# Optimization experiments

Measured on AMD Instinct MI355X. Metric: run time of the kernel, lower is better.

The kernel has to match this reference:

```python
import jax, jax.numpy as jnp
import numpy as np
jax.config.update("jax_enable_x64", True)  # RoPE is applied in float64 in the original

NH, NKV, HD, ROT = 32, 8, 64, 32


def _rope(x, cos, sin):
    # x: [B,h,S,HD]; cos/sin: [B,1,S,ROT//2] (float64)
    x = x.astype(jnp.float64)
    x_rot, x_pass = x[..., :ROT], x[..., ROT:]
    r, i = x_rot[..., :ROT // 2], x_rot[..., ROT // 2:]
    o_r = r * cos - i * sin
    o_i = r * sin + i * cos
    out = jnp.stack((o_r, o_i), axis=-1).reshape(x.shape[:-1] + (ROT,))
    return jnp.concatenate([out, x_pass], axis=-1)


def setup_inputs() -> dict:
    key = jax.random.key(0)
    ks = jax.random.split(key, 16)
    B, S, H, I = 1, 2048, 2048, 8192
    f = jnp.float32
    s = 0.02
    qkv_dim = NH * HD + 2 * NKV * HD  # 3072
    d = {}
    d["hidden_states"] = jax.random.normal(ks[0], (B, S, H), f)
    d["position_ids"] = jnp.arange(B * S, dtype=jnp.int64).reshape(B, S)
    d["cos"] = jax.random.uniform(ks[1], (B, 1, S, ROT // 2), f)
    d["sin"] = jax.random.uniform(ks[2], (B, 1, S, ROT // 2), f)
    d["ln_w"] = jnp.ones((H,), f)
    d["ln_b"] = jnp.zeros((H,), f)
    d["wq"] = jax.random.normal(ks[3], (H, NH * HD), f) * s
    d["wk"] = jax.random.normal(ks[4], (H, NKV * HD), f) * s
    d["wv"] = jax.random.normal(ks[5], (H, NKV * HD), f) * s
    d["wo"] = jax.random.normal(ks[6], (NH * HD, H), f) * s
    d["tau_wq"] = jax.random.normal(ks[7], (qkv_dim, NH), f) * s
    d["tau_wv"] = jax.random.normal(ks[8], (qkv_dim, NH), f) * s
    d["tau_alpha"] = jax.random.normal(ks[9], (NH,), f) * s
    d["up_w"] = jax.random.normal(ks[10], (H, I), f) * s
    d["up_b"] = jnp.zeros((I,), f)
    d["down_w"] = jax.random.normal(ks[11], (I, H), f) * s
    d["down_b"] = jnp.zeros((H,), f)
    return d


def reference(hidden_states, position_ids, cos, sin, ln_w, ln_b, wq, wk, wv, wo,
              tau_wq, tau_wv, tau_alpha, up_w, up_b, down_w, down_b):
    B, S, H = hidden_states.shape
    eps = 1e-5
    # input_layernorm (shared by parallel attn + mlp branches)
    mu = hidden_states.mean(-1, keepdims=True)
    var = hidden_states.var(-1, keepdims=True)
    xn = (hidden_states - mu) / jnp.sqrt(var + eps) * ln_w + ln_b

    # ---- attention with tau gating ----
    q = xn @ wq          # [B,S,NH*HD]
    k = xn @ wk          # [B,S,NKV*HD]
    v = xn @ wv
    qkv = jnp.concatenate([q, k, v], axis=-1)
    tok = jax.nn.gelu(qkv, approximate=False)  # F.gelu default (erf)
    tok_q = jnp.tanh(tok @ tau_wq).transpose(0, 2, 1)  # [B,NH,S]
    tok_v = jnp.tanh(tok @ tau_wv).transpose(0, 2, 1)
    pos = position_ids.astype(tok_q.dtype) + 1
    tau_pos = 1 + (jax.nn.sigmoid(tau_alpha[None, :, None] * jnp.log(pos)[:, None, :]) - 0.5)
    tau_q = (tok_q + tau_pos)[..., None]  # [B,NH,S,1]
    tau_v = (tok_v + tau_pos)[..., None]

    qh = q.reshape(B, S, NH, HD).transpose(0, 2, 1, 3) * tau_q
    kh = k.reshape(B, S, NKV, HD).transpose(0, 2, 1, 3)
    vh = v.reshape(B, S, NKV, HD).transpose(0, 2, 1, 3) * tau_v[:, :NKV]  # repeat-then-slice == first NKV heads

    cos64 = cos.astype(jnp.float64)
    sin64 = sin.astype(jnp.float64)
    qh = _rope(qh, cos64, sin64).astype(jnp.float32)
    kh = _rope(kh, cos64, sin64).astype(jnp.float32)

    g = NH // NKV
    kh = jnp.repeat(kh, g, axis=1)  # GQA expand [B,NKV,S,D] -> [B,NH,S,D]
    vh = jnp.repeat(vh, g, axis=1)

    scores = jnp.einsum('bhqd,bhkd->bhqk', qh, kh) / jnp.sqrt(jnp.float32(HD))
    causal = jnp.tril(jnp.ones((S, S), dtype=bool))
    scores = jnp.where(causal, scores, jnp.float32(-1e9))
    p = jax.nn.softmax(scores, axis=-1)
    attn = jnp.einsum('bhqk,bhkd->bhqd', p, vh)
    attn = attn.transpose(0, 2, 1, 3).reshape(B, S, NH * HD)
    attn_out = attn @ wo

    # ---- dense MLP (gelu_pytorch_tanh, ungated) ----
    h = jax.nn.gelu(xn @ up_w + up_b, approximate=True)
    mlp_out = h @ down_w + down_b

    return hidden_states + attn_out + mlp_out
```

## Files before the change

kernel.cpp:

```cpp
#include <hip/hip_runtime.h>
#include <hip/hip_bf16.h>
#include <math.h>

typedef __bf16 bf16;
typedef bf16 bf16x4 __attribute__((ext_vector_type(4)));
typedef bf16 bf16x8 __attribute__((ext_vector_type(8)));
typedef float f32x4 __attribute__((ext_vector_type(4)));

#define AS1 __attribute__((address_space(1)))
#define AS3 __attribute__((address_space(3)))

__global__ __launch_bounds__(256) void k_transpose(const float* __restrict__ src,
                                                   bf16* __restrict__ dst,
                                                   int R, int C, int dstStride) {
    __shared__ float tile[32][33];
    int bc = blockIdx.x * 32, br = blockIdx.y * 32;
    int tx = threadIdx.x & 31, ty = threadIdx.x >> 5;
    for (int i = 0; i < 4; i++) {
        int r = ty + i * 8;
        tile[r][tx] = src[(size_t)(br + r) * C + bc + tx];
    }
    __syncthreads();
    for (int i = 0; i < 4; i++) {
        int r = ty + i * 8;
        dst[(size_t)(bc + r) * dstStride + br + tx] = (bf16)tile[tx][r];
    }
}

__global__ __launch_bounds__(256) void k_ln(const float* __restrict__ x,
                                            const float* __restrict__ w,
                                            const float* __restrict__ b,
                                            bf16* __restrict__ xn) {
    int s = blockIdx.x;
    int t = threadIdx.x;
    const float* row = x + (size_t)s * 2048;
    const float4* r4 = (const float4*)row;
    float4 A = r4[t * 2], B = r4[t * 2 + 1];
    float sum = A.x + A.y + A.z + A.w + B.x + B.y + B.z + B.w;
    float sq = A.x * A.x + A.y * A.y + A.z * A.z + A.w * A.w +
               B.x * B.x + B.y * B.y + B.z * B.z + B.w * B.w;
    for (int off = 32; off; off >>= 1) {
        sum += __shfl_down(sum, off);
        sq  += __shfl_down(sq, off);
    }
    __shared__ float rs[4], rq[4];
    if ((t & 63) == 0) { rs[t >> 6] = sum; rq[t >> 6] = sq; }
    __syncthreads();
    float S = rs[0] + rs[1] + rs[2] + rs[3];
    float Q = rq[0] + rq[1] + rq[2] + rq[3];
    float mu = S * (1.0f / 2048.0f);
    float var = Q * (1.0f / 2048.0f) - mu * mu;
    float rstd = rsqrtf(var + 1e-5f);
    float vals[8] = {A.x, A.y, A.z, A.w, B.x, B.y, B.z, B.w};
    bf16x8 ov;
    int j0 = t * 8;
    for (int i = 0; i < 8; i++)
        ov[i] = (bf16)((vals[i] - mu) * rstd * w[j0 + i] + b[j0 + i]);
    *(bf16x8*)&xn[(size_t)s * 2048 + j0] = ov;
}

template <int MODE>
__global__ __launch_bounds__(256) void k_gemm(const bf16* __restrict__ A,
                                              const bf16* __restrict__ Bt,
                                              int M, int N, int K, int kslice,
                                              float* __restrict__ Cf,
                                              bf16* __restrict__ Cb,
                                              const float* __restrict__ bias) {
    __shared__ bf16 As[2][128][64];
    __shared__ bf16 Bs[2][128][64];
    int t = threadIdx.x;
    int bm = blockIdx.y, bn = blockIdx.x, bz = blockIdx.z;
    int w = t >> 6, l = t & 63, lr = l & 15, lg = l >> 4;
    int wm = w >> 1, wn = w & 1;
    f32x4 acc[4][4] = {};
    const bf16* Ab = A + (size_t)(bm * 128) * K + (size_t)bz * kslice;
    const bf16* Bb = Bt + (size_t)(bn * 128) * K + (size_t)bz * kslice;
    int srow = t >> 3;
    int scol = ((t & 7) ^ (srow & 7)) * 8;
    int nkt = kslice >> 6;

    auto STAGE = [&](int kt, int buf) {
        int k0 = kt * 64;
#pragma unroll
        for (int i = 0; i < 4; i++) {
            const bf16* ga = Ab + (size_t)(i * 32 + srow) * K + k0 + scol;
            const bf16* gb = Bb + (size_t)(i * 32 + srow) * K + k0 + scol;
            char* la = (char*)(&As[buf][0][0]) + i * 4096 + w * 1024;
            char* lb = (char*)(&Bs[buf][0][0]) + i * 4096 + w * 1024;
            __builtin_amdgcn_global_load_lds(
                (const AS1 void*)ga, (AS3 void*)la, 16, 0, 0);
            __builtin_amdgcn_global_load_lds(
                (const AS1 void*)gb, (AS3 void*)lb, 16, 0, 0);
        }
    };

    int sw = (lr & 7) << 4;

    STAGE(0, 0);
    for (int kt = 0; kt < nkt; ++kt) {
        int cur = kt & 1;
        if (kt + 1 < nkt) {
            STAGE(kt + 1, cur ^ 1);
            asm volatile("s_waitcnt vmcnt(8) lgkmcnt(0)" ::: "memory");
        } else {
            asm volatile("s_waitcnt vmcnt(0) lgkmcnt(0)" ::: "memory");
        }
        __builtin_amdgcn_s_barrier();
        asm volatile("" ::: "memory");
        const char* Abase = (const char*)&As[cur][0][0];
        const char* Bbase = (const char*)&Bs[cur][0][0];
#pragma unroll
        for (int kk = 0; kk < 2; kk++) {
            bf16x8 a[4], b[4];
            for (int fm = 0; fm < 4; fm++)
                a[fm] = *(const bf16x8*)(Abase + (wm * 64 + fm * 16 + lr) * 128 +
                                         ((kk * 64 + lg * 16) ^ sw));
            for (int fn = 0; fn < 4; fn++)
                b[fn] = *(const bf16x8*)(Bbase + (wn * 64 + fn * 16 + lr) * 128 +
                                         ((kk * 64 + lg * 16) ^ sw));
            for (int fm = 0; fm < 4; fm++)
                for (int fn = 0; fn < 4; fn++)
                    acc[fm][fn] = __builtin_amdgcn_mfma_f32_16x16x32_bf16(
                        a[fm], b[fn], acc[fm][fn], 0, 0, 0);
        }
        asm volatile("" ::: "memory");
        __builtin_amdgcn_s_barrier();
    }
    float* Cz = Cf + (size_t)bz * M * N;
    for (int fm = 0; fm < 4; fm++)
        for (int fn = 0; fn < 4; fn++) {
            int col = bn * 128 + wn * 64 + fn * 16 + lr;
            for (int r = 0; r < 4; r++) {
                int row = bm * 128 + wm * 64 + fm * 16 + lg * 4 + r;
                size_t idx = (size_t)row * N + col;
                float v = acc[fm][fn][r];
                if constexpr (MODE == 0) {
                    Cz[idx] = v;
                } else {
                    v += bias[col];
                    float e = __expf(1.5957691216057308f * (v + 0.044715f * v * v * v));
                    float th = 1.0f - 2.0f / (e + 1.0f);
                    Cb[idx] = (bf16)(0.5f * v * (1.0f + th));
                }
            }
        }
}

template <int MODE>
__global__ __launch_bounds__(512, 2) void k_gemm256(const bf16* __restrict__ A,
                                                    const bf16* __restrict__ Bt,
                                                    int M, int N, int K, int kslice,
                                                    float* __restrict__ Cf,
                                                    float* __restrict__ Cf2,
                                                    bf16* __restrict__ Cb,
                                                    const float* __restrict__ bias) {
    __shared__ bf16 As[2][256][64];
    __shared__ bf16 Bs[2][256][64];
    int t = threadIdx.x;
    int w = t >> 6, l = t & 63, lr = l & 15, lg = l >> 4;
    int wm = w >> 2, wn = w & 3;
    int bm = blockIdx.y, bn = blockIdx.x, bz = blockIdx.z;
    f32x4 acc[8][4] = {};
    const bf16* Ab = A + (size_t)(bm * 256) * K + (size_t)bz * kslice;
    const bf16* Bb = Bt + (size_t)(bn * 256) * K + (size_t)bz * kslice;
    int srow = t >> 3;
    int scol = ((t & 7) ^ (srow & 7)) * 8;
    int nkt = kslice >> 6;
    int sw = (lr & 7) << 4;

    auto STAGE = [&](int kt, int buf) {
        int k0 = kt * 64;
#pragma unroll
        for (int i = 0; i < 4; i++) {
            const bf16* ga = Ab + (size_t)(i * 64 + srow) * K + k0 + scol;
            const bf16* gb = Bb + (size_t)(i * 64 + srow) * K + k0 + scol;
            char* la = (char*)(&As[buf][0][0]) + (i * 64 + w * 8) * 128;
            char* lb = (char*)(&Bs[buf][0][0]) + (i * 64 + w * 8) * 128;
            __builtin_amdgcn_global_load_lds(
                (const AS1 void*)ga, (AS3 void*)la, 16, 0, 0);
            __builtin_amdgcn_global_load_lds(
                (const AS1 void*)gb, (AS3 void*)lb, 16, 0, 0);
        }
    };

    STAGE(0, 0);
    asm volatile("s_waitcnt vmcnt(0)" ::: "memory");
    __builtin_amdgcn_s_barrier();
    asm volatile("" ::: "memory");

    for (int kt = 0; kt < nkt; ++kt) {
        int cur = kt & 1;
        const char* Abase = (const char*)&As[cur][0][0] + (wm * 128) * 128;
        const char* Bbase = (const char*)&Bs[cur][0][0] + (wn * 64) * 128;
        bf16x8 a[4][2], b[2][2];
#pragma unroll
        for (int ph = 0; ph < 4; ++ph) {
            const int qm = ph >> 1;
            const int qn = (ph == 1 || ph == 2) ? 1 : 0;
            if (ph == 0 || ph == 2) {
#pragma unroll
                for (int fm = 0; fm < 4; fm++)
#pragma unroll
                    for (int kk = 0; kk < 2; kk++)
                        a[fm][kk] = *(const bf16x8*)(Abase +
                            (qm * 64 + fm * 16 + lr) * 128 +
                            ((kk * 64 + lg * 16) ^ sw));
            }
            if (ph != 2) {
#pragma unroll
                for (int fn = 0; fn < 2; fn++)
#pragma unroll
                    for (int kk = 0; kk < 2; kk++)
                        b[fn][kk] = *(const bf16x8*)(Bbase +
                            (qn * 32 + fn * 16 + lr) * 128 +
                            ((kk * 64 + lg * 16) ^ sw));
            }
            if (ph == 0 && kt + 1 < nkt) STAGE(kt + 1, cur ^ 1);
            __builtin_amdgcn_s_barrier();
            asm volatile("s_waitcnt lgkmcnt(0)" ::: "memory");
            __builtin_amdgcn_sched_barrier(0);
            __builtin_amdgcn_s_setprio(1);
#pragma unroll
            for (int fm = 0; fm < 4; fm++)
#pragma unroll
                for (int fn = 0; fn < 2; fn++)
#pragma unroll
                    for (int kk = 0; kk < 2; kk++)
                        acc[qm * 4 + fm][qn * 2 + fn] =
                            __builtin_amdgcn_mfma_f32_16x16x32_bf16(
                                a[fm][kk], b[fn][kk],
                                acc[qm * 4 + fm][qn * 2 + fn], 0, 0, 0);
            __builtin_amdgcn_s_setprio(0);
            if (ph == 3) asm volatile("s_waitcnt vmcnt(0)" ::: "memory");
            asm volatile("" ::: "memory");
            __builtin_amdgcn_s_barrier();
        }
    }

    float* Cz = ((bz < 2) ? Cf : Cf2) + (size_t)(bz & 1) * M * N;
#pragma unroll
    for (int mi = 0; mi < 8; mi++)
#pragma unroll
        for (int ni = 0; ni < 4; ni++) {
            int col = bn * 256 + wn * 64 + (ni >> 1) * 32 + (ni & 1) * 16 + lr;
            for (int r = 0; r < 4; r++) {
                int row = bm * 256 + wm * 128 + (mi >> 2) * 64 + (mi & 3) * 16 +
                          lg * 4 + r;
                size_t idx = (size_t)row * N + col;
                float v = acc[mi][ni][r];
                if constexpr (MODE == 0) {
                    Cz[idx] = v;
                } else {
                    v += bias[col];
                    float e = __expf(1.5957691216057308f * (v + 0.044715f * v * v * v));
                    float th = 1.0f - 2.0f / (e + 1.0f);
                    Cb[idx] = (bf16)(0.5f * v * (1.0f + th));
                }
            }
        }
}

__global__ __launch_bounds__(256) void k_final(const float* __restrict__ hidden,
                                               const float* __restrict__ w0,
                                               const float* __restrict__ w1,
                                               const float* __restrict__ p0,
                                               const float* __restrict__ p1,
                                               const float* __restrict__ p2,
                                               const float* __restrict__ p3,
                                               const float* __restrict__ bias,
                                               float* __restrict__ out) {
    int idx = blockIdx.x * 256 + threadIdx.x;
    int col4 = idx & 511;
    float4 b = ((const float4*)bias)[col4];
    float4 h = ((const float4*)hidden)[idx];
    float4 a0 = ((const float4*)w0)[idx];
    float4 a1 = ((const float4*)w1)[idx];
    float4 d0 = ((const float4*)p0)[idx];
    float4 d1 = ((const float4*)p1)[idx];
    float4 d2 = ((const float4*)p2)[idx];
    float4 d3 = ((const float4*)p3)[idx];
    float4 o;
    o.x = h.x + a0.x + a1.x + d0.x + d1.x + d2.x + d3.x + b.x;
    o.y = h.y + a0.y + a1.y + d0.y + d1.y + d2.y + d3.y + b.y;
    o.z = h.z + a0.z + a1.z + d0.z + d1.z + d2.z + d3.z + b.z;
    o.w = h.w + a0.w + a1.w + d0.w + d1.w + d2.w + d3.w + b.w;
    ((float4*)out)[idx] = o;
}

__global__ __launch_bounds__(256) void k_tau(const float* __restrict__ qkv,
                                             const float* __restrict__ twq,
                                             const float* __restrict__ twv,
                                             const float* __restrict__ alpha,
                                             const int* __restrict__ pos,
                                             float* __restrict__ tauq,
                                             float* __restrict__ tauv) {
    int s = blockIdx.x;
    __shared__ float tok[3072];
    __shared__ float part[4][64];
    const float* row = qkv + (size_t)s * 3072;
    for (int j = threadIdx.x; j < 3072; j += 256) {
        float x = row[j];
        tok[j] = x * 0.5f * (1.0f + erff(x * 0.7071067811865475f));
    }
    __syncthreads();
    int h = threadIdx.x & 63;
    int chunk = threadIdx.x >> 6;
    const float* W = (h < 32) ? twq : twv;
    int hh = h & 31;
    float acc = 0.0f;
    int j0 = chunk * 768;
    for (int j = j0; j < j0 + 768; ++j) acc += tok[j] * W[j * 32 + hh];
    part[chunk][h] = acc;
    __syncthreads();
    if (chunk == 0) {
        float tot = part[0][h] + part[1][h] + part[2][h] + part[3][h];
        float pf = (float)(pos[s] + 1);
        float lp = logf(pf);
        float tp = 1.0f + (1.0f / (1.0f + expf(-alpha[hh] * lp)) - 0.5f);
        float val = tanhf(tot) + tp;
        if (h < 32) tauq[s * 32 + hh] = val;
        else        tauv[s * 32 + hh] = val;
    }
}

__global__ __launch_bounds__(256) void k_heads(const float* __restrict__ qkv,
                                               const float* __restrict__ cosb,
                                               const float* __restrict__ sinb,
                                               const float* __restrict__ tauq,
                                               const float* __restrict__ tauv,
                                               bf16* __restrict__ Qr,
                                               bf16* __restrict__ Kr,
                                               bf16* __restrict__ Vt) {
    int s = blockIdx.x * 4 + (threadIdx.x >> 6);
    int d = threadIdx.x & 63;
    int j = (d >> 1) & 15;
    float c = cosb[s * 16 + j], sn = sinb[s * 16 + j];
    const float* row = qkv + (size_t)s * 3072;
    for (int h = 0; h < 32; ++h) {
        float x = row[h * 64 + d] * tauq[s * 32 + h] * 0.125f;
        float xr = __shfl(x, j);
        float xi = __shfl(x, j + 16);
        float out = (d < 32) ? ((d & 1) ? (xr * sn + xi * c) : (xr * c - xi * sn)) : x;
        Qr[(size_t)s * 2048 + h * 64 + d] = (bf16)out;
    }
    for (int h = 0; h < 8; ++h) {
        float x = row[2048 + h * 64 + d];
        float xr = __shfl(x, j);
        float xi = __shfl(x, j + 16);
        float out = (d < 32) ? ((d & 1) ? (xr * sn + xi * c) : (xr * c - xi * sn)) : x;
        Kr[(size_t)s * 512 + h * 64 + d] = (bf16)out;
    }
    for (int h = 0; h < 8; ++h) {
        float x = row[2560 + h * 64 + d] * tauv[s * 32 + h];
        Vt[((size_t)h * 64 + d) * 2048 + s] = (bf16)x;
    }
}

__global__ __launch_bounds__(512, 4) void k_attn(const bf16* __restrict__ Q,
                                                 const bf16* __restrict__ K,
                                                 const bf16* __restrict__ Vt,
                                                 bf16* __restrict__ O) {
    __shared__ bf16 Ks[2][64][64];
    __shared__ bf16 Vs[2][64][64];
    __shared__ bf16 plds[8][16][72];
    int t = threadIdx.x;
    int w = t >> 6, l = t & 63, lr = l & 15, lg = l >> 4;
    int h = blockIdx.x, kvh = h >> 2;
    int qb = 15 - blockIdx.y;
    int qrow0 = qb * 128 + w * 16;
    int qg = qrow0 + lr;
    int qmax = qrow0 + 15;
    int nkt = 2 * qb + 2;

    int srow = t >> 3;
    int scol = ((t & 7) * 16) ^ ((srow & 7) << 4);
    const char* gK = (const char*)(K + (size_t)kvh * 64);
    const char* gV = (const char*)(Vt + (size_t)kvh * 64 * 2048);
    char* ldsK = (char*)&Ks[0][0][0] + w * 1024;
    char* ldsV = (char*)&Vs[0][0][0] + w * 1024;

    bf16x8 q0 = *(const bf16x8*)&Q[(size_t)qg * 2048 + h * 64 + lg * 8];
    bf16x8 q1 = *(const bf16x8*)&Q[(size_t)qg * 2048 + h * 64 + 32 + lg * 8];
    f32x4 o[4] = {};
    float m = -3e38f, ll = 0.0f;
    int sw = (lr & 7) << 4;

    __builtin_amdgcn_global_load_lds(
        (const AS1 void*)(gK + (size_t)srow * 1024 + scol), (AS3 void*)ldsK, 16, 0, 0);
    __builtin_amdgcn_global_load_lds(
        (const AS1 void*)(gV + (size_t)srow * 4096 + scol), (AS3 void*)ldsV, 16, 0, 0);
    __syncthreads();

    for (int kt = 0; kt < nkt; ++kt) {
        int kb = kt * 64;
        int cur = kt & 1, nxt = cur ^ 1;
        if (kt + 1 < nkt) {
            int kb2 = kb + 64;
            __builtin_amdgcn_global_load_lds(
                (const AS1 void*)(gK + (size_t)(kb2 + srow) * 1024 + scol),
                (AS3 void*)(ldsK + nxt * 8192), 16, 0, 0);
            __builtin_amdgcn_global_load_lds(
                (const AS1 void*)(gV + (size_t)srow * 4096 + kb2 * 2 + scol),
                (AS3 void*)(ldsV + nxt * 8192), 16, 0, 0);
        }
        if (kb <= qmax) {
            const char* Kbuf = (const char*)Ks + cur * 8192;
            const char* Vbuf = (const char*)Vs + cur * 8192;
            f32x4 sc[2][2];
#pragma unroll
            for (int ks = 0; ks < 2; ks++)
                for (int kc = 0; kc < 2; kc++) {
                    int krow = ks * 32 + kc * 16 + lr;
                    bf16x8 k0 = *(const bf16x8*)(Kbuf + krow * 128 + ((lg * 16) ^ sw));
                    bf16x8 k1 = *(const bf16x8*)(Kbuf + krow * 128 + ((64 + lg * 16) ^ sw));
                    f32x4 z = {};
                    z = __builtin_amdgcn_mfma_f32_16x16x32_bf16(k0, q0, z, 0, 0, 0);
                    sc[ks][kc] = __builtin_amdgcn_mfma_f32_16x16x32_bf16(k1, q1, z, 0, 0, 0);
                }
            if (kb + 63 > qrow0) {
#pragma unroll
                for (int ks = 0; ks < 2; ks++)
                    for (int kc = 0; kc < 2; kc++)
                        for (int r = 0; r < 4; r++) {
                            int kg = kb + ks * 32 + kc * 16 + lg * 4 + r;
                            if (kg > qg) sc[ks][kc][r] = -1e30f;
                        }
            }
            float tmax = -3e38f;
#pragma unroll
            for (int ks = 0; ks < 2; ks++)
                for (int kc = 0; kc < 2; kc++)
                    for (int r = 0; r < 4; r++) tmax = fmaxf(tmax, sc[ks][kc][r]);
            tmax = fmaxf(tmax, __shfl_xor(tmax, 16));
            tmax = fmaxf(tmax, __shfl_xor(tmax, 32));
            if (!__all(tmax <= m)) {
                float mn = fmaxf(m, tmax);
                float al = __expf(m - mn);
                m = mn;
                ll *= al;
#pragma unroll
                for (int fn = 0; fn < 4; fn++)
                    for (int r = 0; r < 4; r++) o[fn][r] *= al;
            }
            float rsum = 0.0f;
#pragma unroll
            for (int ks = 0; ks < 2; ks++)
                for (int kc = 0; kc < 2; kc++) {
                    bf16x4 pk;
                    for (int r = 0; r < 4; r++) {
                        float pv = __expf(sc[ks][kc][r] - m);
                        rsum += pv;
                        pk[r] = (bf16)pv;
                    }
                    *(bf16x4*)&plds[w][lr][ks * 32 + kc * 16 + lg * 4] = pk;
                }
            ll += rsum;
            bf16x8 vf[2][4];
#pragma unroll
            for (int ks = 0; ks < 2; ks++)
                for (int fn = 0; fn < 4; fn++) {
                    int drow = fn * 16 + lr;
                    vf[ks][fn] = *(const bf16x8*)(Vbuf + drow * 128 + ((ks * 64 + lg * 16) ^ sw));
                }
            asm volatile("s_waitcnt lgkmcnt(0)" ::: "memory");
            __builtin_amdgcn_sched_barrier(0);
            bf16x8 pa0 = *(const bf16x8*)&plds[w][lr][lg * 8];
            bf16x8 pa1 = *(const bf16x8*)&plds[w][lr][32 + lg * 8];
#pragma unroll
            for (int fn = 0; fn < 4; fn++)
                o[fn] = __builtin_amdgcn_mfma_f32_16x16x32_bf16(vf[0][fn], pa0, o[fn], 0, 0, 0);
#pragma unroll
            for (int fn = 0; fn < 4; fn++)
                o[fn] = __builtin_amdgcn_mfma_f32_16x16x32_bf16(vf[1][fn], pa1, o[fn], 0, 0, 0);
        }
        __syncthreads();
    }

    ll += __shfl_xor(ll, 16);
    ll += __shfl_xor(ll, 32);
    float rinv = 1.0f / ll;
    for (int fn = 0; fn < 4; fn++) {
        bf16x4 ov;
        for (int r = 0; r < 4; r++) ov[r] = (bf16)(o[fn][r] * rinv);
        *(bf16x4*)&O[(size_t)qg * 2048 + h * 64 + fn * 16 + lg * 4] = ov;
    }
}

extern "C" void kernel_launch(void* const* d_in, const int* in_sizes, int n_in,
                              void* d_out, int out_size, void* d_ws, size_t ws_size,
                              hipStream_t stream) {
    const float* hidden = (const float*)d_in[0];
    const int*   pos    = (const int*)d_in[1];
    const float* cosb   = (const float*)d_in[2];
    const float* sinb   = (const float*)d_in[3];
    const float* ln_w   = (const float*)d_in[4];
    const float* ln_b   = (const float*)d_in[5];
    const float* wq     = (const float*)d_in[6];
    const float* wk     = (const float*)d_in[7];
    const float* wv     = (const float*)d_in[8];
    const float* wo     = (const float*)d_in[9];
    const float* twq    = (const float*)d_in[10];
    const float* twv    = (const float*)d_in[11];
    const float* alpha  = (const float*)d_in[12];
    const float* up_w   = (const float*)d_in[13];
    const float* up_b   = (const float*)d_in[14];
    const float* down_w = (const float*)d_in[15];
    const float* down_b = (const float*)d_in[16];
    float* out = (float*)d_out;

    char* p = (char*)d_ws;
    auto alloc = [&](size_t n) -> char* {
        char* r = p;
        p += (n + 255) & ~(size_t)255;
        return r;
    };
    bf16* wqkvT = (bf16*)alloc((size_t)3072 * 2048 * 2);
    bf16* woT   = (bf16*)alloc((size_t)2048 * 2048 * 2);
    bf16* upT   = (bf16*)alloc((size_t)8192 * 2048 * 2);
    bf16* downT = (bf16*)alloc((size_t)2048 * 8192 * 2);
    bf16* xn    = (bf16*)alloc((size_t)2048 * 2048 * 2);
    float* qkv  = (float*)alloc((size_t)2048 * 3072 * 4);
    float* tauq = (float*)alloc((size_t)2048 * 32 * 4);
    float* tauv = (float*)alloc((size_t)2048 * 32 * 4);
    bf16* Qr    = (bf16*)alloc((size_t)2048 * 2048 * 2);
    bf16* Kr    = (bf16*)alloc((size_t)2048 * 512 * 2);
    bf16* Vt    = (bf16*)alloc((size_t)8 * 64 * 2048 * 2);
    bf16* aout  = (bf16*)alloc((size_t)2048 * 2048 * 2);
    bf16* hbuf  = (bf16*)alloc((size_t)2048 * 8192 * 2);
    float* Wp   = (float*)alloc((size_t)2 * 2048 * 2048 * 4);
    float* Pp   = (float*)alloc((size_t)2 * 2048 * 2048 * 4);
    float* PpX  = qkv;

    k_transpose<<<dim3(64, 64), 256, 0, stream>>>(wq, wqkvT, 2048, 2048, 2048);
    k_transpose<<<dim3(16, 64), 256, 0, stream>>>(wk, wqkvT + (size_t)2048 * 2048, 2048, 512, 2048);
    k_transpose<<<dim3(16, 64), 256, 0, stream>>>(wv, wqkvT + (size_t)2560 * 2048, 2048, 512, 2048);
    k_transpose<<<dim3(64, 64), 256, 0, stream>>>(wo, woT, 2048, 2048, 2048);
    k_transpose<<<dim3(256, 64), 256, 0, stream>>>(up_w, upT, 2048, 8192, 2048);
    k_transpose<<<dim3(64, 256), 256, 0, stream>>>(down_w, downT, 8192, 2048, 8192);

    k_ln<<<2048, 256, 0, stream>>>(hidden, ln_w, ln_b, xn);

    k_gemm<0><<<dim3(24, 16, 1), 256, 0, stream>>>(xn, wqkvT, 2048, 3072, 2048, 2048,
                                                   qkv, nullptr, nullptr);

    k_tau<<<2048, 256, 0, stream>>>(qkv, twq, twv, alpha, pos, tauq, tauv);
    k_heads<<<512, 256, 0, stream>>>(qkv, cosb, sinb, tauq, tauv, Qr, Kr, Vt);

    k_attn<<<dim3(32, 16), 512, 0, stream>>>(Qr, Kr, Vt, aout);

    k_gemm<0><<<dim3(16, 16, 2), 256, 0, stream>>>(aout, woT, 2048, 2048, 2048, 1024,
                                                   Wp, nullptr, nullptr);
    k_gemm256<1><<<dim3(32, 8, 1), 512, 0, stream>>>(xn, upT, 2048, 8192, 2048, 2048,
                                                     nullptr, nullptr, hbuf, up_b);
    k_gemm256<0><<<dim3(8, 8, 4), 512, 0, stream>>>(hbuf, downT, 2048, 2048, 8192, 2048,
                                                    Pp, PpX, nullptr, nullptr);
    k_final<<<4096, 256, 0, stream>>>(hidden, Wp, Wp + (size_t)2048 * 2048,
                                      Pp, Pp + (size_t)2048 * 2048,
                                      PpX, PpX + (size_t)2048 * 2048, down_b, out);
}
```

Baseline: 482.2 us.

## Single-buffer the 128-tile GEMM and stagger 256-tile GEMM prefetch across phases

The 128-tile GEMM drops its LDS double buffer and runs a simple load, wait, sync, compute loop, which halves its shared memory. The 256-tile GEMM splits the next-tile prefetch into four quarter-stages: one is issued at the top of each k-iteration and the other three between MFMA phases. The per-phase barriers, lgkmcnt waits and setprio hints are removed, leaving one barrier per k-iteration. The aim is fewer synchronisations and spread-out memory issue. The risks are lost load/compute overlap in the 128-tile kernel, and a possible LDS overwrite race, because quarter 0 is issued before the barrier that retires reads of that buffer.

```diff
diff --git a/kernel.cpp b/kernel.cpp
--- a/kernel.cpp
+++ b/kernel.cpp
@@ -66,8 +66,8 @@
                                               float* __restrict__ Cf,
                                               bf16* __restrict__ Cb,
                                               const float* __restrict__ bias) {
-    __shared__ bf16 As[2][128][64];
-    __shared__ bf16 Bs[2][128][64];
+    __shared__ bf16 As[128][64];
+    __shared__ bf16 Bs[128][64];
     int t = threadIdx.x;
     int bm = blockIdx.y, bn = blockIdx.x, bz = blockIdx.z;
     int w = t >> 6, l = t & 63, lr = l & 15, lg = l >> 4;
@@ -78,37 +78,26 @@
     int srow = t >> 3;
     int scol = ((t & 7) ^ (srow & 7)) * 8;
     int nkt = kslice >> 6;
-
-    auto STAGE = [&](int kt, int buf) {
+    int sw = (lr & 7) << 4;
+
+    for (int kt = 0; kt < nkt; ++kt) {
         int k0 = kt * 64;
+        if (kt) __syncthreads();
 #pragma unroll
         for (int i = 0; i < 4; i++) {
             const bf16* ga = Ab + (size_t)(i * 32 + srow) * K + k0 + scol;
             const bf16* gb = Bb + (size_t)(i * 32 + srow) * K + k0 + scol;
-            char* la = (char*)(&As[buf][0][0]) + i * 4096 + w * 1024;
-            char* lb = (char*)(&Bs[buf][0][0]) + i * 4096 + w * 1024;
+            char* la = (char*)(&As[0][0]) + i * 4096 + w * 1024;
+            char* lb = (char*)(&Bs[0][0]) + i * 4096 + w * 1024;
             __builtin_amdgcn_global_load_lds(
                 (const AS1 void*)ga, (AS3 void*)la, 16, 0, 0);
             __builtin_amdgcn_global_load_lds(
                 (const AS1 void*)gb, (AS3 void*)lb, 16, 0, 0);
         }
-    };
-
-    int sw = (lr & 7) << 4;
-
-    STAGE(0, 0);
-    for (int kt = 0; kt < nkt; ++kt) {
-        int cur = kt & 1;
-        if (kt + 1 < nkt) {
-            STAGE(kt + 1, cur ^ 1);
-            asm volatile("s_waitcnt vmcnt(8) lgkmcnt(0)" ::: "memory");
-        } else {
-            asm volatile("s_waitcnt vmcnt(0) lgkmcnt(0)" ::: "memory");
-        }
-        __builtin_amdgcn_s_barrier();
-        asm volatile("" ::: "memory");
-        const char* Abase = (const char*)&As[cur][0][0];
-        const char* Bbase = (const char*)&Bs[cur][0][0];
+        asm volatile("s_waitcnt vmcnt(0)" ::: "memory");
+        __syncthreads();
+        const char* Abase = (const char*)&As[0][0];
+        const char* Bbase = (const char*)&Bs[0][0];
 #pragma unroll
         for (int kk = 0; kk < 2; kk++) {
             bf16x8 a[4], b[4];
@@ -123,8 +112,6 @@
                     acc[fm][fn] = __builtin_amdgcn_mfma_f32_16x16x32_bf16(
                         a[fm], b[fn], acc[fm][fn], 0, 0, 0);
         }
-        asm volatile("" ::: "memory");
-        __builtin_amdgcn_s_barrier();
     }
     float* Cz = Cf + (size_t)bz * M * N;
     for (int fm = 0; fm < 4; fm++)
@@ -168,30 +155,41 @@
     int nkt = kslice >> 6;
     int sw = (lr & 7) << 4;
 
-    auto STAGE = [&](int kt, int buf) {
+    auto STAGE_HALF = [&](int kt, int half, int buf) {
         int k0 = kt * 64;
-#pragma unroll
-        for (int i = 0; i < 4; i++) {
-            const bf16* ga = Ab + (size_t)(i * 64 + srow) * K + k0 + scol;
-            const bf16* gb = Bb + (size_t)(i * 64 + srow) * K + k0 + scol;
-            char* la = (char*)(&As[buf][0][0]) + (i * 64 + w * 8) * 128;
-            char* lb = (char*)(&Bs[buf][0][0]) + (i * 64 + w * 8) * 128;
+        const bf16* g = (half < 2) ? Ab : Bb;
+        char* base = (char*)((half < 2) ? &As[buf][0][0] : &Bs[buf][0][0]);
+        int rbase = (half & 1) * 128;
+#pragma unroll
+        for (int i = 0; i < 2; i++) {
+            int row = rbase + i * 64 + srow;
+            const bf16* ga = g + (size_t)row * K + k0 + scol;
+            char* la = base + (rbase + i * 64 + w * 8) * 128;
             __builtin_amdgcn_global_load_lds(
                 (const AS1 void*)ga, (AS3 void*)la, 16, 0, 0);
-            __builtin_amdgcn_global_load_lds(
-                (const AS1 void*)gb, (AS3 void*)lb, 16, 0, 0);
         }
     };
 
-    STAGE(0, 0);
+    for (int h = 0; h < 4; h++) STAGE_HALF(0, h, 0);
     asm volatile("s_waitcnt vmcnt(0)" ::: "memory");
     __builtin_amdgcn_s_barrier();
-    asm volatile("" ::: "memory");
 
     for (int kt = 0; kt < nkt; ++kt) {
-        int cur = kt & 1;
-        const char* Abase = (const char*)&As[cur][0][0] + (wm * 128) * 128;
-        const char* Bbase = (const char*)&Bs[cur][0][0] + (wn * 64) * 128;
+        int buf = kt & 1;
+        bool more = (kt + 1 < nkt);
+        if (kt) {
+            if (more) {
+                STAGE_HALF(kt + 1, 0, buf ^ 1);
+                asm volatile("s_waitcnt vmcnt(2)" ::: "memory");
+            } else {
+                asm volatile("s_waitcnt vmcnt(0)" ::: "memory");
+            }
+            __builtin_amdgcn_s_barrier();
+        } else if (more) {
+            STAGE_HALF(1, 0, 1);
+        }
+        const char* Abase = (const char*)&As[buf][0][0] + (wm * 128) * 128;
+        const char* Bbase = (const char*)&Bs[buf][0][0] + (wn * 64) * 128;
         bf16x8 a[4][2], b[2][2];
 #pragma unroll
         for (int ph = 0; ph < 4; ++ph) {
@@ -215,11 +213,6 @@
                             (qn * 32 + fn * 16 + lr) * 128 +
                             ((kk * 64 + lg * 16) ^ sw));
             }
-            if (ph == 0 && kt + 1 < nkt) STAGE(kt + 1, cur ^ 1);
-            __builtin_amdgcn_s_barrier();
-            asm volatile("s_waitcnt lgkmcnt(0)" ::: "memory");
-            __builtin_amdgcn_sched_barrier(0);
-            __builtin_amdgcn_s_setprio(1);
 #pragma unroll
             for (int fm = 0; fm < 4; fm++)
 #pragma unroll
@@ -230,10 +223,7 @@
                             __builtin_amdgcn_mfma_f32_16x16x32_bf16(
                                 a[fm][kk], b[fn][kk],
                                 acc[qm * 4 + fm][qn * 2 + fn], 0, 0, 0);
-            __builtin_amdgcn_s_setprio(0);
-            if (ph == 3) asm volatile("s_waitcnt vmcnt(0)" ::: "memory");
-            asm volatile("" ::: "memory");
-            __builtin_amdgcn_s_barrier();
+            if (more && ph < 3) STAGE_HALF(kt + 1, ph + 1, buf ^ 1);
         }
     }
 
```

New measurement: 479.3 us. Within noise of the previous version (-0.6%).
